# Kernel optimization log

Measured on AMD Instinct MI355X. Metric: run time of the kernel, lower is better.

Reference implementation:

```python
import jax, jax.numpy as jnp
import numpy as np

N, E, D, H, C, ED = 50000, 800000, 128, 2, 128, 8
LEAKY_SLOPE = 0.2
SOFTMAX_EPS = 1e-16
LN_EPS = 1e-5


def setup_inputs() -> dict:
    key = jax.random.key(0)
    ks = jax.random.split(key, 12)
    s = lambda k, shp, scale: jax.random.normal(k, shp, dtype=jnp.float32) * scale
    return {
        "x": s(ks[0], (N, D), 1.0),
        "edge_index": jax.random.randint(ks[1], (2, E), 0, N, dtype=jnp.int64),
        "edge_attr": s(ks[2], (E, ED), 1.0),
        "W_ep": s(ks[3], (ED, D), 1.0 / np.sqrt(ED)),
        "b_ep": jnp.zeros((D,), jnp.float32),
        "W_lin": s(ks[4], (D, H * C), 1.0 / np.sqrt(D)),
        "att_src": s(ks[5], (H, C), 1.0 / np.sqrt(C)),
        "att_dst": s(ks[6], (H, C), 1.0 / np.sqrt(C)),
        "W_le": s(ks[7], (D, H * C), 1.0 / np.sqrt(D)),
        "att_edge": s(ks[8], (H, C), 1.0 / np.sqrt(C)),
        "bias_gat": jnp.zeros((C,), jnp.float32),
        "ln_gamma": jnp.ones((C,), jnp.float32),
        "ln_beta": jnp.zeros((C,), jnp.float32),
    }


def reference(x, edge_index, edge_attr, W_ep, b_ep, W_lin, att_src, att_dst,
              W_le, att_edge, bias_gat, ln_gamma, ln_beta):
    src, dst = edge_index[0], edge_index[1]
    # edge_proj: [E, ED] -> [E, D]
    e = edge_attr @ W_ep + b_ep
    # node projection: [N, H, C]
    h = (x @ W_lin).reshape(N, H, C)
    # edge projection inside GATConv: [E, H, C]
    ee = (e @ W_le).reshape(E, H, C)
    # attention logits
    a_src = jnp.einsum('nhc,hc->nh', h, att_src)      # [N, H]
    a_dst = jnp.einsum('nhc,hc->nh', h, att_dst)      # [N, H]
    a_edge = jnp.einsum('ehc,hc->eh', ee, att_edge)   # [E, H]
    score = a_src[src] + a_dst[dst] + a_edge          # [E, H]
    score = jnp.where(score >= 0, score, LEAKY_SLOPE * score)
    # segment softmax over incoming edges of each dst node
    smax = jax.ops.segment_max(score, dst, num_segments=N)     # [N, H]
    ex = jnp.exp(score - smax[dst])
    denom = jax.ops.segment_sum(ex, dst, num_segments=N)       # [N, H]
    alpha = ex / (denom[dst] + SOFTMAX_EPS)                    # [E, H]
    # message + scatter-add aggregation
    msg = h[src] * alpha[:, :, None]                           # [E, H, C]
    agg = jax.ops.segment_sum(msg, dst, num_segments=N)        # [N, H, C]
    out = agg.mean(axis=1) + bias_gat                          # concat=False -> head mean
    # residual + LayerNorm (dropout = identity in eval mode)
    y = out + x
    mu = y.mean(axis=-1, keepdims=True)
    var = y.var(axis=-1, keepdims=True)
    return (y - mu) * jax.lax.rsqrt(var + LN_EPS) * ln_gamma + ln_beta
```

## Files before the change

kernel.cpp:

```cpp
#include <hip/hip_runtime.h>
#include <hip/hip_bf16.h>

#define NN 50000
#define EE 800000
#define DD 128
#define HH 2
#define CC 128
#define HC 256
#define EDD 8

#define LEAKY 0.2f
#define SMEPS 1e-16f
#define LNEPS 1e-5f

#define SCAN_B 196
#define CONV_B 3125
#define K2_B   782
#define NPAD   50176

#define HB_OFF    0u
#define ASRC_OFF  12800000u
#define ADST_OFF  13200000u
#define CONST_OFF 13600000u
#define SD_OFF    13604096u
#define CNT8_OFF  20004096u
#define ROW_OFF   21609728u
#define BASE8_OFF 21810432u
#define PAY_OFF   23416064u
#define WBT_OFF   29816064u
#define BSUM_OFF  29881600u

typedef __attribute__((ext_vector_type(8))) short short8v;
typedef __attribute__((ext_vector_type(4))) float float4v;
typedef __attribute__((ext_vector_type(2))) int int2v;

__device__ __forceinline__ float bf2f(unsigned short v) {
  return __uint_as_float(((unsigned)v) << 16);
}
__device__ __forceinline__ unsigned short f2bf(float f) {
  __hip_bfloat16 b = __float2bfloat16(f);
  return *reinterpret_cast<unsigned short*>(&b);
}

__global__ __launch_bounds__(256) void k1_prep(const float* __restrict__ W_lin,
                                               const float* __restrict__ att_src,
                                               const float* __restrict__ att_dst,
                                               const float* __restrict__ W_le,
                                               const float* __restrict__ att_edge,
                                               const float* __restrict__ W_ep,
                                               const float* __restrict__ b_ep,
                                               float* __restrict__ consts,
                                               unsigned short* __restrict__ wbT,
                                               int* __restrict__ cnt8) {
  int b = blockIdx.x, tid = threadIdx.x;
  if (b == 0) {
    __shared__ float vlds[HH * DD];
    int h = tid >> 7, d = tid & 127;
    const float* as = att_src + h * CC;
    const float* ad = att_dst + h * CC;
    const float* ae = att_edge + h * CC;
    float us = 0.f, ud = 0.f, vv = 0.f;
    for (int c = 0; c < CC; ++c) {
      float wl = W_lin[d * HC + h * CC + c];
      float we = W_le[d * HC + h * CC + c];
      us += wl * as[c]; ud += wl * ad[c]; vv += we * ae[c];
    }
    consts[h * 128 + d] = us;
    consts[256 + h * 128 + d] = ud;
    vlds[h * 128 + d] = vv;
    __syncthreads();
    if (tid < 16) {
      int hh = tid >> 3, k = tid & 7;
      float w = 0.f;
      for (int dd2 = 0; dd2 < DD; ++dd2) w += W_ep[k * DD + dd2] * vlds[hh * 128 + dd2];
      consts[512 + hh * 8 + k] = w;
    }
    if (tid < 2) {
      float ce = 0.f;
      for (int dd2 = 0; dd2 < DD; ++dd2) ce += b_ep[dd2] * vlds[tid * 128 + dd2];
      consts[528 + tid] = ce;
    }
  } else if (b <= 128) {
    int i = (b - 1) * 256 + tid;
    int k = i >> 8, c = i & 255;
    wbT[c * DD + k] = f2bf(W_lin[i]);
  } else {
    int n = (b - 129) * 256 + tid;
#pragma unroll
    for (int r = 0; r < 8; ++r) cnt8[r * NPAD + n] = 0;
  }
}

__global__ __launch_bounds__(256) void k2_conv_mfma(const float* __restrict__ x,
                                                    const unsigned short* __restrict__ wbT,
                                                    const float* __restrict__ consts,
                                                    const int* __restrict__ ei_raw,
                                                    unsigned char* __restrict__ hbuf8,
                                                    float* __restrict__ a_src,
                                                    float* __restrict__ a_dst,
                                                    int* __restrict__ cnt8,
                                                    int2v* __restrict__ sd) {
  __shared__ unsigned short xs[64 * 256];
  int tid = threadIdx.x;

  if (blockIdx.x >= K2_B) {
    int lane = tid & 63;
    int probe = ei_raw[2 * lane + 1];
    bool is64 = (__ballot(probe != 0) == 0ull);
    int xcd = __builtin_amdgcn_s_getreg((20) | (0 << 6) | ((32 - 1) << 11)) & 7;
    int i = (blockIdx.x - K2_B) * 256 + tid;
    int s, d;
    if (is64) { s = ei_raw[2 * i]; d = ei_raw[2 * (EE + i)]; }
    else      { s = ei_raw[i];     d = ei_raw[EE + i]; }
    int rk = __hip_atomic_fetch_add(&cnt8[xcd * NPAD + d], 1,
                                    __ATOMIC_RELAXED, __HIP_MEMORY_SCOPE_WORKGROUP);
    int2v v; v.x = s; v.y = d | (rk << 16) | (xcd << 29);
    sd[i] = v;
    return;
  }

  int n0 = blockIdx.x * 64;
  int r = tid >> 2, q = tid & 3;
  int n = n0 + r;
  bool valid = (n < NN);

  float xv[32];
  const float4* xp = (const float4*)(x + (size_t)n * DD + q * 32);
#pragma unroll
  for (int j = 0; j < 8; ++j) {
    float4 v = valid ? xp[j] : make_float4(0.f, 0.f, 0.f, 0.f);
    xv[j * 4 + 0] = v.x; xv[j * 4 + 1] = v.y; xv[j * 4 + 2] = v.z; xv[j * 4 + 3] = v.w;
  }
  float ps0 = 0.f, ps1 = 0.f, pd0 = 0.f, pd1 = 0.f;
#pragma unroll
  for (int j = 0; j < 32; j += 4) {
    float4 u0 = *(const float4*)(consts +   0 + q * 32 + j);
    float4 u1 = *(const float4*)(consts + 128 + q * 32 + j);
    float4 v0 = *(const float4*)(consts + 256 + q * 32 + j);
    float4 v1 = *(const float4*)(consts + 384 + q * 32 + j);
    ps0 += xv[j] * u0.x + xv[j+1] * u0.y + xv[j+2] * u0.z + xv[j+3] * u0.w;
    ps1 += xv[j] * u1.x + xv[j+1] * u1.y + xv[j+2] * u1.z + xv[j+3] * u1.w;
    pd0 += xv[j] * v0.x + xv[j+1] * v0.y + xv[j+2] * v0.z + xv[j+3] * v0.w;
    pd1 += xv[j] * v1.x + xv[j+1] * v1.y + xv[j+2] * v1.z + xv[j+3] * v1.w;
  }
#pragma unroll
  for (int off = 1; off < 4; off <<= 1) {
    ps0 += __shfl_xor(ps0, off); ps1 += __shfl_xor(ps1, off);
    pd0 += __shfl_xor(pd0, off); pd1 += __shfl_xor(pd1, off);
  }
  if (q == 0 && valid) {
    *(float2*)(a_src + n * 2) = make_float2(ps0, ps1);
    *(float2*)(a_dst + n * 2) = make_float2(pd0, pd1);
  }

#pragma unroll
  for (int ci = 0; ci < 4; ++ci) {
    union { short8v v; unsigned short u[8]; } pk;
#pragma unroll
    for (int j = 0; j < 8; ++j) pk.u[j] = f2bf(xv[ci * 8 + j]);
    unsigned byte = r * 256 + (q * 4 + ci) * 16;
    byte ^= (r & 7) << 4;
    *(short8v*)((char*)xs + byte) = pk.v;
  }

  int wave = tid >> 6, l = tid & 63;
  int wc = wave * 64;
  int lr = l & 15, lg = l >> 4;
  short8v bfr[4][4];
#pragma unroll
  for (int ct = 0; ct < 4; ++ct) {
    int col = wc + ct * 16 + lr;
#pragma unroll
    for (int kt = 0; kt < 4; ++kt)
      bfr[ct][kt] = *(const short8v*)(wbT + (size_t)col * DD + kt * 32 + lg * 8);
  }

  __syncthreads();

  float4v acc[4][4];
#pragma unroll
  for (int rt = 0; rt < 4; ++rt)
#pragma unroll
    for (int ct = 0; ct < 4; ++ct) acc[rt][ct] = (float4v){0.f, 0.f, 0.f, 0.f};

#pragma unroll
  for (int kt = 0; kt < 4; ++kt) {
    short8v afr[4];
#pragma unroll
    for (int rt = 0; rt < 4; ++rt) {
      int row = rt * 16 + lr;
      unsigned byte = row * 256 + kt * 64 + lg * 16;
      byte ^= (row & 7) << 4;
      afr[rt] = *(const short8v*)((const char*)xs + byte);
    }
#pragma unroll
    for (int rt = 0; rt < 4; ++rt)
#pragma unroll
      for (int ct = 0; ct < 4; ++ct)
        acc[rt][ct] = __builtin_amdgcn_mfma_f32_16x16x32_bf16(afr[rt], bfr[ct][kt], acc[rt][ct], 0, 0, 0);
  }

  __syncthreads();
#pragma unroll
  for (int rt = 0; rt < 4; ++rt) {
#pragma unroll
    for (int j = 0; j < 4; ++j) {
      int row = rt * 16 + lg * 4 + j;
#pragma unroll
      for (int ct = 0; ct < 4; ++ct) {
        int col = wc + ct * 16 + lr;
        int idx2 = ((col & 127) << 1) | (col >> 7);
        unsigned o = (unsigned)idx2 * 2;
        unsigned byte = row * 512 + (o ^ ((((unsigned)(row & 7) ^ ((o >> 7) & 3))) << 4));
        *(unsigned short*)((char*)xs + byte) = f2bf(acc[rt][ct][j]);
      }
    }
  }
  __syncthreads();
  {
    int r2 = tid >> 2, q2 = tid & 3;
    int n2 = n0 + r2;
    if (n2 < NN) {
#pragma unroll
      for (int kk = 0; kk < 4; ++kk) {
        unsigned u4[4];
#pragma unroll
        for (int t2 = 0; t2 < 2; ++t2) {
          int k = kk * 2 + t2;
          unsigned o = q2 * 128 + k * 16;
          unsigned byte = r2 * 512 + (o ^ ((((unsigned)(r2 & 7) ^ ((o >> 7) & 3))) << 4));
          short8v v = *(short8v*)((char*)xs + byte);
          unsigned ua = __builtin_amdgcn_cvt_pk_fp8_f32(bf2f((unsigned short)v[0]), bf2f((unsigned short)v[1]), 0u, false);
          ua = __builtin_amdgcn_cvt_pk_fp8_f32(bf2f((unsigned short)v[2]), bf2f((unsigned short)v[3]), ua, true);
          unsigned ub = __builtin_amdgcn_cvt_pk_fp8_f32(bf2f((unsigned short)v[4]), bf2f((unsigned short)v[5]), 0u, false);
          ub = __builtin_amdgcn_cvt_pk_fp8_f32(bf2f((unsigned short)v[6]), bf2f((unsigned short)v[7]), ub, true);
          u4[t2 * 2] = ua; u4[t2 * 2 + 1] = ub;
        }
        uint4 w4 = make_uint4(u4[0], u4[1], u4[2], u4[3]);
        *(uint4*)(hbuf8 + (size_t)n2 * 256 + q2 * 64 + kk * 16) = w4;
      }
    }
  }
}

__global__ __launch_bounds__(256) void k_scan1(const int* __restrict__ cnt8,
                                               int* __restrict__ rowstart,
                                               int* __restrict__ base8,
                                               int* __restrict__ bsum) {
  __shared__ int sp[256];
  int t = threadIdx.x, b = blockIdx.x;
  int n = b * 256 + t;
  int c[8];
  int tot = 0;
#pragma unroll
  for (int r = 0; r < 8; ++r) {
    c[r] = (n < NN) ? cnt8[r * NPAD + n] : 0;
    tot += c[r];
  }
  sp[t] = tot;
  __syncthreads();
  for (int off = 1; off < 256; off <<= 1) {
    int u = (t >= off) ? sp[t - off] : 0;
    __syncthreads();
    sp[t] += u;
    __syncthreads();
  }
  int intra = sp[t] - tot;
  if (n < NN) {
    rowstart[n] = intra;
    int run = intra;
#pragma unroll
    for (int r = 0; r < 8; ++r) { base8[r * NPAD + n] = run; run += c[r]; }
  }
  if (t == 255) bsum[b] = sp[255];
}

__global__ __launch_bounds__(256) void k34_edge(const int2v* __restrict__ sd,
                                                const int* __restrict__ base8,
                                                const int* __restrict__ bsum,
                                                const float* __restrict__ edge_attr,
                                                const float* __restrict__ a_src,
                                                const float* __restrict__ a_dst,
                                                const float* __restrict__ consts,
                                                int2v* __restrict__ payload) {
  __shared__ int bs[256];
  int t = threadIdx.x;
  {
    int v = (t < SCAN_B) ? bsum[t] : 0;
    bs[t] = v;
    __syncthreads();
    for (int off = 1; off < 256; off <<= 1) {
      int u = (t >= off) ? bs[t - off] : 0;
      __syncthreads();
      bs[t] += u;
      __syncthreads();
    }
  }
  int e = blockIdx.x * 256 + t;
  int2v sdv = sd[e];
  int s = sdv.x;
  unsigned y = (unsigned)sdv.y;
  int d = (int)(y & 0xFFFFu);
  int rk = (int)((y >> 16) & 0x1FFFu);
  int xcd = (int)(y >> 29);
  float4 ea0 = *(const float4*)(edge_attr + (size_t)e * 8);
  float4 ea1 = *(const float4*)(edge_attr + (size_t)e * 8 + 4);
  float2 asv = *(const float2*)(a_src + s * 2);
  float2 adv = *(const float2*)(a_dst + d * 2);
  const float* w0 = consts + 512;
  const float* w1 = consts + 520;
  float sc0 = asv.x + adv.x + consts[528]
            + ea0.x * w0[0] + ea0.y * w0[1] + ea0.z * w0[2] + ea0.w * w0[3]
            + ea1.x * w0[4] + ea1.y * w0[5] + ea1.z * w0[6] + ea1.w * w0[7];
  float sc1 = asv.y + adv.y + consts[529]
            + ea0.x * w1[0] + ea0.y * w1[1] + ea0.z * w1[2] + ea0.w * w1[3]
            + ea1.x * w1[4] + ea1.y * w1[5] + ea1.z * w1[6] + ea1.w * w1[7];
  sc0 = (sc0 >= 0.f) ? sc0 : LEAKY * sc0;
  sc1 = (sc1 >= 0.f) ? sc1 : LEAKY * sc1;
  float ex0 = __expf(sc0);
  float ex1 = __expf(sc1);
  unsigned pk = (unsigned)f2bf(ex0) | ((unsigned)f2bf(ex1) << 16);
  int blk = d >> 8;
  int boff = (blk == 0) ? 0 : bs[blk - 1];
  int pos = base8[xcd * NPAD + d] + boff + rk;
  int2v pv; pv.x = s << 8; pv.y = (int)pk;
  payload[pos] = pv;
}

__global__ __launch_bounds__(256) void k5_fused(const int* __restrict__ rowstart,
                                                const int* __restrict__ bsum,
                                                const int2v* __restrict__ payload,
                                                const unsigned char* __restrict__ hb8,
                                                const float* __restrict__ x,
                                                const float* __restrict__ bias,
                                                const float* __restrict__ gamma,
                                                const float* __restrict__ beta,
                                                float* __restrict__ out) {
  __shared__ int bs[256];
  int t = threadIdx.x;
  {
    int v = (t < SCAN_B) ? bsum[t] : 0;
    bs[t] = v;
    __syncthreads();
    for (int off = 1; off < 256; off <<= 1) {
      int u = (t >= off) ? bs[t - off] : 0;
      __syncthreads();
      bs[t] += u;
      __syncthreads();
    }
  }
  int n = blockIdx.x * 4 + (t >> 6);
  int lane = t & 63;
  int b0 = n >> 8;
  int p0i = rowstart[n] + ((b0 == 0) ? 0 : bs[b0 - 1]);
  int p1i;
  if (n + 1 == NN) p1i = EE;
  else {
    int b1 = (n + 1) >> 8;
    p1i = rowstart[n + 1] + ((b1 == 0) ? 0 : bs[b1 - 1]);
  }
  p0i = __builtin_amdgcn_readfirstlane(p0i);
  p1i = __builtin_amdgcn_readfirstlane(p1i);
  int len = p1i - p0i;
  int c0 = lane * 2;
  const int2v* pp = payload + p0i;
  float a00 = 0.f, a01 = 0.f, a10 = 0.f, a11 = 0.f, se0 = 0.f, se1 = 0.f;

#define K5_LD(soff) (*(const unsigned*)(hb8 + (size_t)(unsigned)(soff) + lane * 4))
#define K5_ACC(pl, w) { \
    float ex0 = bf2f((unsigned short)((unsigned)(pl).y & 0xffffu)); \
    float ex1 = bf2f((unsigned short)(((unsigned)(pl).y) >> 16)); \
    a00 = fmaf(ex0, __builtin_amdgcn_cvt_f32_fp8((int)(w), 0), a00); \
    a01 = fmaf(ex1, __builtin_amdgcn_cvt_f32_fp8((int)(w), 1), a01); \
    a10 = fmaf(ex0, __builtin_amdgcn_cvt_f32_fp8((int)(w), 2), a10); \
    a11 = fmaf(ex1, __builtin_amdgcn_cvt_f32_fp8((int)(w), 3), a11); \
    se0 += ex0; se1 += ex1; }

  if (len > 0) {
    int2v p0 = pp[0];
    int2v p1 = (len > 1) ? pp[1] : p0;
    int2v p2 = (len > 2) ? pp[2] : p0;
    int2v p3 = (len > 3) ? pp[3] : p0;
    unsigned h0 = K5_LD(p0.x), h1 = K5_LD(p1.x), h2 = K5_LD(p2.x), h3 = K5_LD(p3.x);
    int i = 0;
    for (; i + 7 < len; i += 4) {
      int2v q0 = pp[i + 4], q1 = pp[i + 5], q2 = pp[i + 6], q3 = pp[i + 7];
      unsigned g0 = K5_LD(q0.x), g1 = K5_LD(q1.x), g2 = K5_LD(q2.x), g3 = K5_LD(q3.x);
      K5_ACC(p0, h0); K5_ACC(p1, h1); K5_ACC(p2, h2); K5_ACC(p3, h3);
      p0 = q0; p1 = q1; p2 = q2; p3 = q3;
      h0 = g0; h1 = g1; h2 = g2; h3 = g3;
    }
    int r = len - i;
    K5_ACC(p0, h0);
    if (r > 1) K5_ACC(p1, h1);
    if (r > 2) K5_ACC(p2, h2);
    if (r > 3) K5_ACC(p3, h3);
    if (r > 4) {
      int rem = r - 4;
      int2v q0 = pp[i + 4];
      int2v q1 = (rem > 1) ? pp[i + 5] : q0;
      int2v q2 = (rem > 2) ? pp[i + 6] : q0;
      unsigned g0 = K5_LD(q0.x), g1 = K5_LD(q1.x), g2 = K5_LD(q2.x);
      K5_ACC(q0, g0);
      if (rem > 1) K5_ACC(q1, g1);
      if (rem > 2) K5_ACC(q2, g2);
    }
  }
#undef K5_LD
#undef K5_ACC

  float inv0 = 0.5f / (se0 + SMEPS);
  float inv1 = 0.5f / (se1 + SMEPS);
  float2 xv = *(const float2*)(x + (size_t)n * DD + c0);
  float v0 = a00 * inv0 + a01 * inv1 + bias[c0] + xv.x;
  float v1 = a10 * inv0 + a11 * inv1 + bias[c0 + 1] + xv.y;
  float s = v0 + v1, ss = v0 * v0 + v1 * v1;
#pragma unroll
  for (int o = 32; o > 0; o >>= 1) {
    s += __shfl_xor(s, o);
    ss += __shfl_xor(ss, o);
  }
  float mu = s * (1.f / 128.f);
  float var = ss * (1.f / 128.f) - mu * mu;
  float rstd = rsqrtf(var + LNEPS);
  float2 ov;
  ov.x = (v0 - mu) * rstd * gamma[c0] + beta[c0];
  ov.y = (v1 - mu) * rstd * gamma[c0 + 1] + beta[c0 + 1];
  *(float2*)(out + (size_t)n * CC + c0) = ov;
}

extern "C" void kernel_launch(void* const* d_in, const int* in_sizes, int n_in,
                              void* d_out, int out_size, void* d_ws, size_t ws_size,
                              hipStream_t stream) {
  const float* x        = (const float*)d_in[0];
  const int*   ei_raw   = (const int*)d_in[1];
  const float* edge_attr= (const float*)d_in[2];
  const float* W_ep     = (const float*)d_in[3];
  const float* b_ep     = (const float*)d_in[4];
  const float* W_lin    = (const float*)d_in[5];
  const float* att_src  = (const float*)d_in[6];
  const float* att_dst  = (const float*)d_in[7];
  const float* W_le     = (const float*)d_in[8];
  const float* att_edge = (const float*)d_in[9];
  const float* bias_gat = (const float*)d_in[10];
  const float* ln_gamma = (const float*)d_in[11];
  const float* ln_beta  = (const float*)d_in[12];

  char* ws = (char*)d_ws;
  unsigned char* hbuf8 = (unsigned char*)(ws + HB_OFF);
  float*    a_src  = (float*)(ws + ASRC_OFF);
  float*    a_dst  = (float*)(ws + ADST_OFF);
  float*    consts = (float*)(ws + CONST_OFF);
  int2v*    sd     = (int2v*)(ws + SD_OFF);
  int*      cnt8   = (int*)(ws + CNT8_OFF);
  int*      rowst  = (int*)(ws + ROW_OFF);
  int*      base8  = (int*)(ws + BASE8_OFF);
  int2v*    payload= (int2v*)(ws + PAY_OFF);
  unsigned short* wbT = (unsigned short*)(ws + WBT_OFF);
  int*      bsum   = (int*)(ws + BSUM_OFF);

  k1_prep<<<325, 256, 0, stream>>>(W_lin, att_src, att_dst, W_le, att_edge, W_ep, b_ep,
                                   consts, wbT, cnt8);
  k2_conv_mfma<<<K2_B + CONV_B, 256, 0, stream>>>(x, wbT, consts, ei_raw, hbuf8,
                                                  a_src, a_dst, cnt8, sd);
  k_scan1<<<SCAN_B, 256, 0, stream>>>(cnt8, rowst, base8, bsum);
  k34_edge<<<CONV_B, 256, 0, stream>>>(sd, base8, bsum, edge_attr, a_src, a_dst, consts, payload);
  k5_fused<<<NN / 4, 256, 0, stream>>>(rowst, bsum, payload, hbuf8, x, bias_gat, ln_gamma, ln_beta, (float*)d_out);
}
```

Before: 144.7 us.

## Regroup kernels: fuse edge-count atomics into prep and scan into MFMA conv

The stage boundaries are reshuffled. The per-edge destination counting and rank atomics move into the prep kernel, and the per-block count scan is merged with the node projection MFMA kernel as extra blocks. Zeroing of the counters moves to a hipMemsetAsync ahead of the prep kernel. Kernel launches drop from three to two plus a memset, and the scan now overlaps with the node GEMM instead of running as a small serial launch. The trade-off is that the memset adds its own stream operation.

```diff
diff --git a/kernel.cpp b/kernel.cpp
--- a/kernel.cpp
+++ b/kernel.cpp
@@ -42,16 +42,18 @@
   return *reinterpret_cast<unsigned short*>(&b);
 }
 
-__global__ __launch_bounds__(256) void k1_prep(const float* __restrict__ W_lin,
-                                               const float* __restrict__ att_src,
-                                               const float* __restrict__ att_dst,
-                                               const float* __restrict__ W_le,
-                                               const float* __restrict__ att_edge,
-                                               const float* __restrict__ W_ep,
-                                               const float* __restrict__ b_ep,
-                                               float* __restrict__ consts,
-                                               unsigned short* __restrict__ wbT,
-                                               int* __restrict__ cnt8) {
+__global__ __launch_bounds__(256) void kA_prep_convert(const float* __restrict__ W_lin,
+                                                       const float* __restrict__ att_src,
+                                                       const float* __restrict__ att_dst,
+                                                       const float* __restrict__ W_le,
+                                                       const float* __restrict__ att_edge,
+                                                       const float* __restrict__ W_ep,
+                                                       const float* __restrict__ b_ep,
+                                                       const int* __restrict__ ei_raw,
+                                                       float* __restrict__ consts,
+                                                       unsigned short* __restrict__ wbT,
+                                                       int* __restrict__ cnt8,
+                                                       int2v* __restrict__ sd) {
   int b = blockIdx.x, tid = threadIdx.x;
   if (b == 0) {
     __shared__ float vlds[HH * DD];
@@ -85,30 +87,11 @@
     int k = i >> 8, c = i & 255;
     wbT[c * DD + k] = f2bf(W_lin[i]);
   } else {
-    int n = (b - 129) * 256 + tid;
-#pragma unroll
-    for (int r = 0; r < 8; ++r) cnt8[r * NPAD + n] = 0;
-  }
-}
-
-__global__ __launch_bounds__(256) void k2_conv_mfma(const float* __restrict__ x,
-                                                    const unsigned short* __restrict__ wbT,
-                                                    const float* __restrict__ consts,
-                                                    const int* __restrict__ ei_raw,
-                                                    unsigned char* __restrict__ hbuf8,
-                                                    float* __restrict__ a_src,
-                                                    float* __restrict__ a_dst,
-                                                    int* __restrict__ cnt8,
-                                                    int2v* __restrict__ sd) {
-  __shared__ unsigned short xs[64 * 256];
-  int tid = threadIdx.x;
-
-  if (blockIdx.x >= K2_B) {
     int lane = tid & 63;
     int probe = ei_raw[2 * lane + 1];
     bool is64 = (__ballot(probe != 0) == 0ull);
     int xcd = __builtin_amdgcn_s_getreg((20) | (0 << 6) | ((32 - 1) << 11)) & 7;
-    int i = (blockIdx.x - K2_B) * 256 + tid;
+    int i = (b - 129) * 256 + tid;
     int s, d;
     if (is64) { s = ei_raw[2 * i]; d = ei_raw[2 * (EE + i)]; }
     else      { s = ei_raw[i];     d = ei_raw[EE + i]; }
@@ -116,10 +99,53 @@
                                     __ATOMIC_RELAXED, __HIP_MEMORY_SCOPE_WORKGROUP);
     int2v v; v.x = s; v.y = d | (rk << 16) | (xcd << 29);
     sd[i] = v;
+  }
+}
+
+__global__ __launch_bounds__(256) void kB_scan_mfma(const int* __restrict__ cnt8,
+                                                    int* __restrict__ rowstart,
+                                                    int* __restrict__ base8,
+                                                    int* __restrict__ bsum,
+                                                    const float* __restrict__ x,
+                                                    const unsigned short* __restrict__ wbT,
+                                                    const float* __restrict__ consts,
+                                                    unsigned char* __restrict__ hbuf8,
+                                                    float* __restrict__ a_src,
+                                                    float* __restrict__ a_dst) {
+  __shared__ unsigned short xs[64 * 256];
+  int tid = threadIdx.x;
+
+  if (blockIdx.x < SCAN_B) {
+    int* sp = (int*)xs;
+    int t = tid, b = blockIdx.x;
+    int n = b * 256 + t;
+    int c[8];
+    int tot = 0;
+#pragma unroll
+    for (int r = 0; r < 8; ++r) {
+      c[r] = (n < NN) ? cnt8[r * NPAD + n] : 0;
+      tot += c[r];
+    }
+    sp[t] = tot;
+    __syncthreads();
+    for (int off = 1; off < 256; off <<= 1) {
+      int u = (t >= off) ? sp[t - off] : 0;
+      __syncthreads();
+      sp[t] += u;
+      __syncthreads();
+    }
+    int intra = sp[t] - tot;
+    if (n < NN) {
+      rowstart[n] = intra;
+      int run = intra;
+#pragma unroll
+      for (int r = 0; r < 8; ++r) { base8[r * NPAD + n] = run; run += c[r]; }
+    }
+    if (t == 255) bsum[b] = sp[255];
     return;
   }
 
-  int n0 = blockIdx.x * 64;
+  int n0 = (blockIdx.x - SCAN_B) * 64;
   int r = tid >> 2, q = tid & 3;
   int n = n0 + r;
   bool valid = (n < NN);
@@ -241,38 +267,6 @@
       }
     }
   }
-}
-
-__global__ __launch_bounds__(256) void k_scan1(const int* __restrict__ cnt8,
-                                               int* __restrict__ rowstart,
-                                               int* __restrict__ base8,
-                                               int* __restrict__ bsum) {
-  __shared__ int sp[256];
-  int t = threadIdx.x, b = blockIdx.x;
-  int n = b * 256 + t;
-  int c[8];
-  int tot = 0;
-#pragma unroll
-  for (int r = 0; r < 8; ++r) {
-    c[r] = (n < NN) ? cnt8[r * NPAD + n] : 0;
-    tot += c[r];
-  }
-  sp[t] = tot;
-  __syncthreads();
-  for (int off = 1; off < 256; off <<= 1) {
-    int u = (t >= off) ? sp[t - off] : 0;
-    __syncthreads();
-    sp[t] += u;
-    __syncthreads();
-  }
-  int intra = sp[t] - tot;
-  if (n < NN) {
-    rowstart[n] = intra;
-    int run = intra;
-#pragma unroll
-    for (int r = 0; r < 8; ++r) { base8[r * NPAD + n] = run; run += c[r]; }
-  }
-  if (t == 255) bsum[b] = sp[255];
 }
 
 __global__ __launch_bounds__(256) void k34_edge(const int2v* __restrict__ sd,
@@ -459,11 +453,11 @@
   unsigned short* wbT = (unsigned short*)(ws + WBT_OFF);
   int*      bsum   = (int*)(ws + BSUM_OFF);
 
-  k1_prep<<<325, 256, 0, stream>>>(W_lin, att_src, att_dst, W_le, att_edge, W_ep, b_ep,
-                                   consts, wbT, cnt8);
-  k2_conv_mfma<<<K2_B + CONV_B, 256, 0, stream>>>(x, wbT, consts, ei_raw, hbuf8,
-                                                  a_src, a_dst, cnt8, sd);
-  k_scan1<<<SCAN_B, 256, 0, stream>>>(cnt8, rowst, base8, bsum);
+  hipMemsetAsync(cnt8, 0, (size_t)8 * NPAD * 4, stream);
+  kA_prep_convert<<<129 + CONV_B, 256, 0, stream>>>(W_lin, att_src, att_dst, W_le, att_edge,
+                                                    W_ep, b_ep, ei_raw, consts, wbT, cnt8, sd);
+  kB_scan_mfma<<<SCAN_B + K2_B, 256, 0, stream>>>(cnt8, rowst, base8, bsum,
+                                                  x, wbT, consts, hbuf8, a_src, a_dst);
   k34_edge<<<CONV_B, 256, 0, stream>>>(sd, base8, bsum, edge_attr, a_src, a_dst, consts, payload);
   k5_fused<<<NN / 4, 256, 0, stream>>>(rowst, bsum, payload, hbuf8, x, bias_gat, ln_gamma, ln_beta, (float*)d_out);
 }
```

Result: slower. 148.5 us (+2.6%).
